# Kernel optimization log

Measured on AMD Instinct MI355X. Metric: run time of the kernel, lower is better.

The kernel has to match this reference:

```python
import jax, jax.numpy as jnp
import numpy as np
from jax.scipy.special import logsumexp

B, L = 32, 128
NEG = -1e9
SPAN_LAMB = 0.5


def setup_inputs() -> dict:
    key = jax.random.key(0)
    ks = jax.random.split(key, 8)
    span_logits = jax.random.normal(ks[0], (B, L, L, 2), jnp.float32)
    ph = jax.random.normal(ks[1], (B, L, L), jnp.float32)
    pt = jax.random.normal(ks[2], (B, L, L), jnp.float32)
    ph_arc = jax.random.normal(ks[3], (B, L, L), jnp.float32)
    spans_ind = jax.random.randint(ks[4], (B, L, L), 0, 3, jnp.int32)
    ph_ind = jax.random.randint(ks[5], (B, L, L), 0, 2, jnp.int32)
    pt_ind = jax.random.randint(ks[6], (B, L, L), 0, 2, jnp.int32)
    lens = jax.random.randint(ks[7], (B,), L // 2, L + 1, jnp.int32)
    i = jnp.arange(L)
    # maskspan[b,i,j] = valid right-closed span i..j within sentence b; row 0 sums to lens
    maskspan = (i[None, :, None] <= i[None, None, :]) & (i[None, None, :] < lens[:, None, None])
    maskarc = (i[None, :, None] < lens[:, None, None]) & (i[None, None, :] < lens[:, None, None])
    return dict(span_logits=span_logits, ph=ph, pt=pt, ph_arc=ph_arc,
                spans_ind=spans_ind, ph_ind=ph_ind, pt_ind=pt_ind,
                maskspan=maskspan, maskarc=maskarc)


def _inside_logZ(span_logits, lens):
    # CYK inside algorithm over right-closed spans; returns sum_b logZ_b.
    scores = logsumexp(span_logits, axis=-1)  # [B,L,L] span score = lse over labels
    Ln = scores.shape[1]
    ar = jnp.arange(Ln)
    # width-0 base: s[i,i] = scores[i,i]
    s0 = jnp.where(jnp.eye(Ln, dtype=bool)[None], scores, NEG)
    li = ar[:, None] + ar[None, :]        # [L,L]: left child right end i+k
    ri = li + 1                           # right child left end i+k+1
    li_c = jnp.clip(li, 0, Ln - 1)
    ri_c = jnp.clip(ri, 0, Ln - 1)

    def step(s, w):
        j = ar + w
        jc = jnp.clip(j, 0, Ln - 1)
        left = s[:, ar[:, None], li_c]                 # [B,L,L] left[b,i,k]=s[b,i,i+k]
        right = s[:, ri_c, jc[:, None]]                # right[b,i,k]=s[b,i+k+1,i+w]
        comb = jnp.where(ar[None, None, :] < w, left + right, NEG)
        new = scores[:, ar, jc] + logsumexp(comb, axis=-1)  # [B,L]
        valid = (j < Ln)[None, :]
        cur = s[:, ar, jc]
        s = s.at[:, ar, jc].set(jnp.where(valid, new, cur))
        return s, None

    s, _ = jax.lax.scan(step, s0, jnp.arange(1, Ln))
    logZ = jnp.take_along_axis(s[:, 0, :], (lens - 1)[:, None], axis=1)[:, 0]
    return logZ.sum()


def _bce_mean(x, y, m):
    # stable BCEWithLogits, mean over masked elements
    l = jnp.maximum(x, 0.0) - x * y + jnp.log1p(jnp.exp(-jnp.abs(x)))
    return jnp.where(m, l, 0.0).sum() / m.sum().astype(jnp.float32)


def reference(span_logits, ph, pt, ph_arc, spans_ind, ph_ind, pt_ind, maskspan, maskarc):
    lens = maskspan[:, 0].sum(-1)                         # [B]
    spans_b = jnp.where(spans_ind > 0, spans_ind - 1, spans_ind).astype(bool)
    # label marginals = d logZ / d span_logits (matches torch autograd-based cyk)
    marginals = jax.grad(_inside_logZ)(span_logits, lens)  # [B,L,L,2]
    pos_mask = maskspan & spans_b
    neg_mask = maskspan & (~spans_b)
    pos_loss = jnp.log(jnp.where(pos_mask, jnp.maximum(marginals[..., 1], 1e-38), 1.0)).sum()
    neg_loss = jnp.log(jnp.where(neg_mask, jnp.maximum(marginals[..., 0], 1e-38), 1.0)).sum()
    loss_spans = -(pos_loss + neg_loss) / lens.sum().astype(jnp.float32)
    loss_ph = _bce_mean(ph, ph_ind.astype(jnp.float32), maskarc)
    loss_pt = _bce_mean(pt, pt_ind.astype(jnp.float32), maskarc)
    return SPAN_LAMB * loss_spans + (1.0 - SPAN_LAMB) * (loss_ph + loss_pt)
```

## Files before the change

### kernel.cpp

```cpp
#include <hip/hip_runtime.h>
#include <hip/hip_bf16.h>
#include <float.h>

#define NB 32
#define NBCE 32
#define L 128
#define NT 1024
#define R 132
#define PAD 40
#define LOGMIN -87.49823f

__device__ __forceinline__ int mask_mode(const void* p) {
    unsigned int v = ((const unsigned int*)p)[0];
    if (v == 1u) return 1;
    if (v == 0x3F800000u) return 2;
    return 0;
}
__device__ __forceinline__ bool mask_at(const void* p, int mode, int idx) {
    if (mode == 1) return ((const int*)p)[idx] != 0;
    if (mode == 2) return ((const float*)p)[idx] != 0.0f;
    return ((const unsigned char*)p)[idx] != 0;
}

__device__ __forceinline__ float lse2(float a, float b) {
    return fmaxf(a, b) + log1pf(__expf(-fabsf(a - b)));
}

template<int C>
__device__ __forceinline__ float dppf(float x) {
    return __int_as_float(__builtin_amdgcn_mov_dpp(__float_as_int(x), C, 0xF, 0xF, true));
}
template<int T>
__device__ __forceinline__ float bfly_max(float x) {
    x = fmaxf(x, dppf<0xB1>(x));
    x = fmaxf(x, dppf<0x4E>(x));
    x = fmaxf(x, dppf<0x141>(x));
    if (T == 16) x = fmaxf(x, dppf<0x140>(x));
    return x;
}
template<int T>
__device__ __forceinline__ float bfly_add(float x) {
    x += dppf<0xB1>(x);
    x += dppf<0x4E>(x);
    x += dppf<0x141>(x);
    if (T == 16) x += dppf<0x140>(x);
    return x;
}

template<int T, int NUMAX>
__device__ __forceinline__ void load_terms(float* v, int sub, int nterm,
                                           const float* p1, const float* p2, float& mloc) {
    p1 += sub; p2 += sub;
#pragma unroll
    for (int kk = 0; kk < NUMAX; kk += 2) {
        if (kk * T >= nterm) break;
        const int o0 = kk * T, o1 = o0 + T;
        float a0 = p1[o0] + p2[o0];
        float a1 = p1[o1] + p2[o1];
        a0 = (sub + o0 < nterm) ? a0 : -FLT_MAX;
        a1 = (sub + o1 < nterm) ? a1 : -FLT_MAX;
        v[kk] = a0; v[kk + 1] = a1;
        mloc = fmaxf(mloc, fmaxf(a0, a1));
    }
}
template<int T, int NUMAX>
__device__ __forceinline__ void sum_exp(const float* v, int nterm, float M, float& s) {
#pragma unroll
    for (int kk = 0; kk < NUMAX; kk += 2) {
        if (kk * T >= nterm) break;
        s += __expf(v[kk] - M) + __expf(v[kk + 1] - M);
    }
}

__global__ __launch_bounds__(NT, 1) void tree_dp_kernel(
    const float* __restrict__ logits,
    const int*   __restrict__ spans_ind,
    const void*  __restrict__ maskspan,
    const float* __restrict__ ph, const float* __restrict__ pt,
    const int* __restrict__ ph_ind, const int* __restrict__ pt_ind,
    const void* __restrict__ maskarc,
    double*      __restrict__ ws)
{
    const int tid = threadIdx.x;

    if (blockIdx.x >= NB) {
        const int mode = mask_mode(maskarc);
        const int tot = NB * L * L;
        double sph = 0.0, spt = 0.0, cnt = 0.0;
        for (int idx = (blockIdx.x - NB) * NT + tid; idx < tot; idx += NBCE * NT) {
            if (mask_at(maskarc, mode, idx)) {
                float x = ph[idx]; float y = (float)ph_ind[idx];
                sph += (double)(fmaxf(x, 0.0f) - x * y + log1pf(__expf(-fabsf(x))));
                x = pt[idx]; y = (float)pt_ind[idx];
                spt += (double)(fmaxf(x, 0.0f) - x * y + log1pf(__expf(-fabsf(x))));
                cnt += 1.0;
            }
        }
        for (int off = 32; off > 0; off >>= 1) {
            sph += __shfl_down(sph, off);
            spt += __shfl_down(spt, off);
            cnt += __shfl_down(cnt, off);
        }
        if ((tid & 63) == 0) {
            atomicAdd(&ws[2], sph); atomicAdd(&ws[3], spt); atomicAdd(&ws[4], cnt);
        }
        return;
    }

    __shared__ float Am[L * R + PAD];
    __shared__ float Gm[L * R + PAD];

    const int b = blockIdx.x;
    const int mbase = b * L * L;
    const int mode = mask_mode(maskspan);

    int pred = (tid < L) && mask_at(maskspan, mode, mbase + tid);
    const int n = __syncthreads_count(pred);

    const float* lg = logits + (size_t)b * L * L * 2;

    for (int e = tid; e < L * L; e += NT) {
        int i = e >> 7, j = e & (L - 1);
        if (i <= j && j < n) {
            const float* p = lg + (size_t)e * 2;
            float v = lse2(p[0], p[1]);
            Am[i * R + j] = v; Am[j * R + i] = v;
            Gm[i * R + j] = v; Gm[j * R + i] = v;
        }
    }
    __syncthreads();

    for (int w = 1; w < n; ++w) {
        int c = n - w;
        if (c > 64) {
            int cell = tid >> 3, sub = tid & 7;
            if (cell < c) {
                int i = cell, j = i + w;
                float v[8]; float mloc = -FLT_MAX;
                load_terms<8, 8>(v, sub, w, &Am[i * R + i], &Am[j * R + i + 1], mloc);
                float M = bfly_max<8>(mloc);
                float s = 0.0f;
                sum_exp<8, 8>(v, w, M, s);
                float S = bfly_add<8>(s);
                if (sub == 0) {
                    float val = Am[i * R + j] + M + __logf(S);
                    Am[i * R + j] = val; Am[j * R + i] = val;
                }
            }
        } else {
            int cell = tid >> 4, sub = tid & 15;
            if (cell < c) {
                int i = cell, j = i + w;
                float v[8]; float mloc = -FLT_MAX;
                load_terms<16, 8>(v, sub, w, &Am[i * R + i], &Am[j * R + i + 1], mloc);
                float M = bfly_max<16>(mloc);
                float s = 0.0f;
                sum_exp<16, 8>(v, w, M, s);
                float S = bfly_add<16>(s);
                if (sub == 0) {
                    float val = Am[i * R + j] + M + __logf(S);
                    Am[i * R + j] = val; Am[j * R + i] = val;
                }
            }
        }
        __syncthreads();
    }

    const float logZ = Am[n - 1];

    for (int w = n - 2; w >= 1; --w) {
        int c = n - w;
        if (c > 64) {
            int cell = tid >> 3, sub = tid & 7;
            if (cell < c) {
                int i = cell, j = i + w;
                int nt1 = n - 1 - j;
                float v1[16], v2[16]; float mloc = -FLT_MAX;
                load_terms<8, 16>(v1, sub, nt1, &Gm[i * R + j + 1], &Am[(j + 1) * R + j + 1], mloc);
                load_terms<8, 16>(v2, sub, i,   &Gm[j * R],         &Am[(i - 1) * R],         mloc);
                float M = bfly_max<8>(mloc);
                float s = 0.0f;
                sum_exp<8, 16>(v1, nt1, M, s);
                sum_exp<8, 16>(v2, i,   M, s);
                float S = bfly_add<8>(s);
                if (sub == 0) {
                    float val = Gm[i * R + j] + M + __logf(S);
                    Gm[i * R + j] = val; Gm[j * R + i] = val;
                }
            }
        } else {
            int cell = tid >> 4, sub = tid & 15;
            if (cell < c) {
                int i = cell, j = i + w;
                int nt1 = n - 1 - j;
                float v1[4], v2[4]; float mloc = -FLT_MAX;
                load_terms<16, 4>(v1, sub, nt1, &Gm[i * R + j + 1], &Am[(j + 1) * R + j + 1], mloc);
                load_terms<16, 4>(v2, sub, i,   &Gm[j * R],         &Am[(i - 1) * R],         mloc);
                float M = bfly_max<16>(mloc);
                float s = 0.0f;
                sum_exp<16, 4>(v1, nt1, M, s);
                sum_exp<16, 4>(v2, i,   M, s);
                float S = bfly_add<16>(s);
                if (sub == 0) {
                    float val = Gm[i * R + j] + M + __logf(S);
                    Gm[i * R + j] = val; Gm[j * R + i] = val;
                }
            }
        }
        __syncthreads();
    }

    const int* si = spans_ind + mbase;
    double local = 0.0;
    {
        int cell = tid >> 3, sub = tid & 7;
        if (cell < n) {
            int i = cell;
            int nt1 = n - 1 - i;
            float v1[16], v2[16]; float mloc = -FLT_MAX;
            load_terms<8, 16>(v1, sub, nt1, &Gm[i * R + i + 1], &Am[(i + 1) * R + i + 1], mloc);
            load_terms<8, 16>(v2, sub, i,   &Gm[i * R],         &Am[(i - 1) * R],         mloc);
            float M = bfly_max<8>(mloc);
            float s = 0.0f;
            sum_exp<8, 16>(v1, nt1, M, s);
            sum_exp<8, 16>(v2, i,   M, s);
            float S = bfly_add<8>(s);
            if (sub == 0) {
                float beta_ii = M + __logf(S);
                const float* p = lg + ((size_t)i * L + i) * 2;
                int ind = si[i * L + i];
                float lc = (ind == 2) ? p[1] : p[0];
                float logm = beta_ii - logZ + lc;
                local += (double)fmaxf(logm, LOGMIN);
            }
        }
    }

    for (int e = tid; e < L * L; e += NT) {
        int i = e >> 7, j = e & (L - 1);
        if (i < j && j < n) {
            const float* p = lg + (size_t)e * 2;
            float a = p[0], cc = p[1];
            float sc = lse2(a, cc);
            int ind = si[e];
            float lc = (ind == 2) ? cc : a;
            float logm = Am[i * R + j] + Gm[i * R + j] - logZ + lc - 2.0f * sc;
            local += (double)fmaxf(logm, LOGMIN);
        }
    }

    for (int off = 32; off > 0; off >>= 1)
        local += __shfl_down(local, off);
    if ((tid & 63) == 0) atomicAdd(&ws[0], local);
    if (tid == 0) atomicAdd(&ws[1], (double)n);
}

__global__ void finalize_kernel(const double* __restrict__ ws, float* __restrict__ out) {
    double loss_spans = -ws[0] / ws[1];
    double bce = (ws[2] + ws[3]) / ws[4];
    out[0] = (float)(0.5 * loss_spans + 0.5 * bce);
}

extern "C" void kernel_launch(void* const* d_in, const int* in_sizes, int n_in,
                              void* d_out, int out_size, void* d_ws, size_t ws_size,
                              hipStream_t stream) {
    (void)in_sizes; (void)n_in; (void)out_size; (void)ws_size;
    const float* span_logits = (const float*)d_in[0];
    const float* ph          = (const float*)d_in[1];
    const float* pt          = (const float*)d_in[2];
    const int*   spans_ind   = (const int*)d_in[4];
    const int*   ph_ind      = (const int*)d_in[5];
    const int*   pt_ind      = (const int*)d_in[6];
    const void*  maskspan    = d_in[7];
    const void*  maskarc     = d_in[8];
    double* ws = (double*)d_ws;
    float* out = (float*)d_out;

    hipMemsetAsync(d_ws, 0, 5 * sizeof(double), stream);
    hipLaunchKernelGGL(tree_dp_kernel, dim3(NB + NBCE), dim3(NT), 0, stream,
                       span_logits, spans_ind, maskspan,
                       ph, pt, ph_ind, pt_ind, maskarc, ws);
    hipLaunchKernelGGL(finalize_kernel, dim3(1), dim3(1), 0, stream, ws, out);
}
```

Before: 323.7 us.

## Tile CYK inside/outside passes into 16x16 diagonal blocks with per-wave wavefront

Replaces the per-width global sweep (one block-wide barrier per span width, about n barriers each for inside and outside) with a 16x16 tiled schedule. For each tile diagonal, the split points outside the tile are reduced in bulk into a shared float2 buffer holding online-logsumexp pairs. Each wave then finishes its own tile with an intra-tile wavefront of 31 steps, using online max/sum merges and 4-lane DPP butterflies. This cuts block-level synchronizations to roughly 2·n/16, at the cost of more intra-wave serialized steps, extra shared memory, and changed floating-point summation order.

```diff
diff --git a/kernel.cpp b/kernel.cpp
--- a/kernel.cpp
+++ b/kernel.cpp
@@ -8,6 +8,7 @@
 #define NT 1024
 #define R 132
 #define PAD 40
+#define MAXD 8
 #define LOGMIN -87.49823f
 
 __device__ __forceinline__ int mask_mode(const void* p) {
@@ -26,9 +27,26 @@
     return fmaxf(a, b) + log1pf(__expf(-fabsf(a - b)));
 }
 
+__device__ __forceinline__ void lse_acc(float v, float& m, float& s) {
+    float nm = fmaxf(m, v);
+    s = s * __expf(m - nm) + __expf(v - nm);
+    m = nm;
+}
+__device__ __forceinline__ void lse_merge(float& m1, float& s1, float m2, float s2) {
+    float M = fmaxf(m1, m2);
+    s1 = s1 * __expf(m1 - M) + s2 * __expf(m2 - M);
+    m1 = M;
+}
+
 template<int C>
 __device__ __forceinline__ float dppf(float x) {
     return __int_as_float(__builtin_amdgcn_mov_dpp(__float_as_int(x), C, 0xF, 0xF, true));
+}
+__device__ __forceinline__ void bfly4_lse(float& m, float& s) {
+    float mo = dppf<0xB1>(m), so = dppf<0xB1>(s);
+    lse_merge(m, s, mo, so);
+    mo = dppf<0x4E>(m); so = dppf<0x4E>(s);
+    lse_merge(m, s, mo, so);
 }
 template<int T>
 __device__ __forceinline__ float bfly_max(float x) {
@@ -46,7 +64,6 @@
     if (T == 16) x += dppf<0x140>(x);
     return x;
 }
-
 template<int T, int NUMAX>
 __device__ __forceinline__ void load_terms(float* v, int sub, int nterm,
                                            const float* p1, const float* p2, float& mloc) {
@@ -109,6 +126,7 @@
 
     __shared__ float Am[L * R + PAD];
     __shared__ float Gm[L * R + PAD];
+    __shared__ float2 EB[MAXD * 256];
 
     const int b = blockIdx.x;
     const int mbase = b * L * L;
@@ -116,6 +134,7 @@
 
     int pred = (tid < L) && mask_at(maskspan, mode, mbase + tid);
     const int n = __syncthreads_count(pred);
+    const int D = (n + 15) >> 4;
 
     const float* lg = logits + (size_t)b * L * L * 2;
 
@@ -130,80 +149,145 @@
     }
     __syncthreads();
 
-    for (int w = 1; w < n; ++w) {
-        int c = n - w;
-        if (c > 64) {
-            int cell = tid >> 3, sub = tid & 7;
-            if (cell < c) {
-                int i = cell, j = i + w;
-                float v[8]; float mloc = -FLT_MAX;
-                load_terms<8, 8>(v, sub, w, &Am[i * R + i], &Am[j * R + i + 1], mloc);
-                float M = bfly_max<8>(mloc);
-                float s = 0.0f;
-                sum_exp<8, 8>(v, w, M, s);
-                float S = bfly_add<8>(s);
-                if (sub == 0) {
-                    float val = Am[i * R + j] + M + __logf(S);
-                    Am[i * R + j] = val; Am[j * R + i] = val;
-                }
-            }
-        } else {
-            int cell = tid >> 4, sub = tid & 15;
-            if (cell < c) {
-                int i = cell, j = i + w;
-                float v[8]; float mloc = -FLT_MAX;
-                load_terms<16, 8>(v, sub, w, &Am[i * R + i], &Am[j * R + i + 1], mloc);
-                float M = bfly_max<16>(mloc);
-                float s = 0.0f;
-                sum_exp<16, 8>(v, w, M, s);
-                float S = bfly_add<16>(s);
-                if (sub == 0) {
-                    float val = Am[i * R + j] + M + __logf(S);
-                    Am[i * R + j] = val; Am[j * R + i] = val;
-                }
-            }
+    const int wave = tid >> 6, lane = tid & 63;
+    const int cid4 = lane >> 2, sub4 = lane & 3;
+
+    if (wave < D) {
+        const int bI = wave << 4;
+        for (int lw = 1; lw < 16; ++lw) {
+            int li = cid4, lj = li + lw;
+            int i = bI + li, j = bI + lj;
+            bool act = (lj < 16) && (j < n);
+            float m0 = -FLT_MAX, s0 = 0.f;
+            if (act) {
+                const float* pL = Am + i * R + i;
+                const float* pR = Am + j * R + i + 1;
+                for (int t = sub4; t < lw; t += 4)
+                    lse_acc(pL[t] + pR[t], m0, s0);
+            }
+            bfly4_lse(m0, s0);
+            if (act && sub4 == 0) {
+                float v = Am[i * R + j] + m0 + __logf(s0);
+                Am[i * R + j] = v; Am[j * R + i] = v;
+            }
+        }
+    }
+    __syncthreads();
+
+    for (int d = 1; d < D; ++d) {
+        const int TD = D - d;
+        for (int cidx = tid; cidx < (TD << 8); cidx += NT) {
+            int It = cidx >> 8, c = cidx & 255;
+            int li = c >> 4, lj = c & 15;
+            int i = (It << 4) + li, j = ((It + d) << 4) + lj;
+            float m0 = -FLT_MAX, s0 = 0.f, m1 = -FLT_MAX, s1 = 0.f;
+            if (j < n) {
+                int mlo = (It << 4) + 15;
+                int cnt = (d << 4) - 15;
+                const float* p1 = Am + i * R + mlo;
+                const float* p2 = Am + j * R + mlo + 1;
+                int t = 0;
+                for (; t + 1 < cnt; t += 2) {
+                    lse_acc(p1[t] + p2[t], m0, s0);
+                    lse_acc(p1[t + 1] + p2[t + 1], m1, s1);
+                }
+                if (t < cnt) lse_acc(p1[t] + p2[t], m0, s0);
+                lse_merge(m0, s0, m1, s1);
+            }
+            EB[cidx] = make_float2(m0, s0);
         }
         __syncthreads();
+        if (wave < TD) {
+            const int bI = wave << 4, bJ = (wave + d) << 4;
+            const int ebase = wave << 8;
+            for (int step = 0; step < 31; ++step) {
+                int delta = step - 15;
+                int li = (delta >= 0) ? cid4 : (cid4 - delta);
+                int lj = li + delta;
+                int i = bI + li, j = bJ + lj;
+                bool act = (li < 16) && (lj < 16) && (j < n);
+                float m0 = -FLT_MAX, s0 = 0.f, m1 = -FLT_MAX, s1 = 0.f;
+                if (act) {
+                    const float* rI = Am + i * R;
+                    const float* rJ = Am + j * R;
+                    int nL = lj, nR = 15 - li;
+                    for (int t = sub4; t < nL; t += 4)
+                        lse_acc(rI[bJ + t] + rJ[bJ + 1 + t], m0, s0);
+                    for (int t = sub4; t < nR; t += 4)
+                        lse_acc(rI[bI + li + t] + rJ[bI + li + 1 + t], m1, s1);
+                    lse_merge(m0, s0, m1, s1);
+                }
+                bfly4_lse(m0, s0);
+                if (act && sub4 == 0) {
+                    float2 e = EB[ebase + (li << 4) + lj];
+                    lse_merge(m0, s0, e.x, e.y);
+                    float v = Am[i * R + j] + m0 + __logf(s0);
+                    Am[i * R + j] = v; Am[j * R + i] = v;
+                }
+            }
+        }
+        __syncthreads();
     }
 
     const float logZ = Am[n - 1];
 
-    for (int w = n - 2; w >= 1; --w) {
-        int c = n - w;
-        if (c > 64) {
-            int cell = tid >> 3, sub = tid & 7;
-            if (cell < c) {
-                int i = cell, j = i + w;
-                int nt1 = n - 1 - j;
-                float v1[16], v2[16]; float mloc = -FLT_MAX;
-                load_terms<8, 16>(v1, sub, nt1, &Gm[i * R + j + 1], &Am[(j + 1) * R + j + 1], mloc);
-                load_terms<8, 16>(v2, sub, i,   &Gm[j * R],         &Am[(i - 1) * R],         mloc);
-                float M = bfly_max<8>(mloc);
-                float s = 0.0f;
-                sum_exp<8, 16>(v1, nt1, M, s);
-                sum_exp<8, 16>(v2, i,   M, s);
-                float S = bfly_add<8>(s);
-                if (sub == 0) {
-                    float val = Gm[i * R + j] + M + __logf(S);
-                    Gm[i * R + j] = val; Gm[j * R + i] = val;
-                }
-            }
-        } else {
-            int cell = tid >> 4, sub = tid & 15;
-            if (cell < c) {
-                int i = cell, j = i + w;
-                int nt1 = n - 1 - j;
-                float v1[4], v2[4]; float mloc = -FLT_MAX;
-                load_terms<16, 4>(v1, sub, nt1, &Gm[i * R + j + 1], &Am[(j + 1) * R + j + 1], mloc);
-                load_terms<16, 4>(v2, sub, i,   &Gm[j * R],         &Am[(i - 1) * R],         mloc);
-                float M = bfly_max<16>(mloc);
-                float s = 0.0f;
-                sum_exp<16, 4>(v1, nt1, M, s);
-                sum_exp<16, 4>(v2, i,   M, s);
-                float S = bfly_add<16>(s);
-                if (sub == 0) {
-                    float val = Gm[i * R + j] + M + __logf(S);
-                    Gm[i * R + j] = val; Gm[j * R + i] = val;
+    for (int d = D - 1; d >= 0; --d) {
+        const int TD = D - d;
+        for (int cidx = tid; cidx < (TD << 8); cidx += NT) {
+            int It = cidx >> 8, c = cidx & 255;
+            int li = c >> 4, lj = c & 15;
+            int I = It, J = It + d;
+            int i = (I << 4) + li, j = (J << 4) + lj;
+            float m0 = -FLT_MAX, s0 = 0.f, m1 = -FLT_MAX, s1 = 0.f;
+            if (j < n) {
+                int k0 = (J + 1) << 4;
+                int nEA = n - k0; if (nEA < 0) nEA = 0;
+                int t = 0;
+                for (; t + 1 < nEA; t += 2) {
+                    lse_acc(Gm[i * R + k0 + t] + Am[(j + 1) * R + k0 + t], m0, s0);
+                    lse_acc(Gm[i * R + k0 + t + 1] + Am[(j + 1) * R + k0 + t + 1], m1, s1);
+                }
+                if (t < nEA) lse_acc(Gm[i * R + k0 + t] + Am[(j + 1) * R + k0 + t], m0, s0);
+                int nEB_ = I << 4;
+                t = 0;
+                for (; t + 1 < nEB_; t += 2) {
+                    lse_acc(Gm[j * R + t] + Am[(i - 1) * R + t], m0, s0);
+                    lse_acc(Gm[j * R + t + 1] + Am[(i - 1) * R + t + 1], m1, s1);
+                }
+                if (t < nEB_) lse_acc(Gm[j * R + t] + Am[(i - 1) * R + t], m0, s0);
+                lse_merge(m0, s0, m1, s1);
+            }
+            EB[cidx] = make_float2(m0, s0);
+        }
+        __syncthreads();
+        if (wave < TD) {
+            const int bI = wave << 4, bJ = (wave + d) << 4;
+            const int ebase = wave << 8;
+            const int stepLo = (d == 0) ? 16 : 0;
+            for (int step = 30; step >= stepLo; --step) {
+                int delta = step - 15;
+                int li = (delta >= 0) ? cid4 : (cid4 - delta);
+                int lj = li + delta;
+                int i = bI + li, j = bJ + lj;
+                bool act = (li < 16) && (lj < 16) && (j < n);
+                float m0 = -FLT_MAX, s0 = 0.f, m1 = -FLT_MAX, s1 = 0.f;
+                if (act) {
+                    int nA = 15 - lj; { int lim = n - 1 - j; if (nA > lim) nA = lim; }
+                    int nB = li;
+                    for (int t = sub4; t < nA; t += 4)
+                        lse_acc(Gm[i * R + j + 1 + t] + Am[(j + 1) * R + j + 1 + t], m0, s0);
+                    for (int t = sub4; t < nB; t += 4)
+                        lse_acc(Gm[j * R + bI + t] + Am[(i - 1) * R + bI + t], m1, s1);
+                    lse_merge(m0, s0, m1, s1);
+                }
+                bfly4_lse(m0, s0);
+                if (act && sub4 == 0) {
+                    float2 e = EB[ebase + (li << 4) + lj];
+                    lse_merge(m0, s0, e.x, e.y);
+                    if (s0 > 0.f) {
+                        float v = Gm[i * R + j] + m0 + __logf(s0);
+                        Gm[i * R + j] = v; Gm[j * R + i] = v;
+                    }
                 }
             }
         }
@@ -235,7 +319,6 @@
             }
         }
     }
-
     for (int e = tid; e < L * L; e += NT) {
         int i = e >> 7, j = e & (L - 1);
         if (i < j && j < n) {
@@ -248,7 +331,6 @@
             local += (double)fmaxf(logm, LOGMIN);
         }
     }
-
     for (int off = 32; off > 0; off >>= 1)
         local += __shfl_down(local, off);
     if ((tid & 63) == 0) atomicAdd(&ws[0], local);
```

After: 551.9 us. 70.5% more time.

## Overlap wavefront steps by deferring edge-dependent terms past the barrier

Applied to the files above, without the earlier changes.

Each step of the inside and outside wavefronts now reduces only the terms that do not depend on the previous width before the barrier. The two boundary terms that read cells from the immediately preceding width are folded in afterwards with an online log-sum-exp update. That leaves one barrier per width while letting most of the reduction for width w run alongside the tail writes of width w-1. The risk is subtle ordering bugs, since the post-barrier writes of one step race with the pre-barrier reads of the next step.

```diff
diff --git a/kernel.cpp b/kernel.cpp
--- a/kernel.cpp
+++ b/kernel.cpp
@@ -26,6 +26,12 @@
     return fmaxf(a, b) + log1pf(__expf(-fabsf(a - b)));
 }
 
+__device__ __forceinline__ void lse_acc(float v, float& m, float& s) {
+    float nm = fmaxf(m, v);
+    s = s * __expf(m - nm) + __expf(v - nm);
+    m = nm;
+}
+
 template<int C>
 __device__ __forceinline__ float dppf(float x) {
     return __int_as_float(__builtin_amdgcn_mov_dpp(__float_as_int(x), C, 0xF, 0xF, true));
@@ -46,7 +52,6 @@
     if (T == 16) x += dppf<0x140>(x);
     return x;
 }
-
 template<int T, int NUMAX>
 __device__ __forceinline__ void load_terms(float* v, int sub, int nterm,
                                            const float* p1, const float* p2, float& mloc) {
@@ -130,85 +135,116 @@
     }
     __syncthreads();
 
-    for (int w = 1; w < n; ++w) {
+    if (tid < n - 1) {
+        int i = tid, j = i + 1;
+        float val = Am[i * R + j] + Am[i * R + i] + Am[j * R + j];
+        Am[i * R + j] = val; Am[j * R + i] = val;
+    }
+
+    for (int w = 2; w < n; ++w) {
         int c = n - w;
+        float M = -FLT_MAX, S = 0.0f;
+        float pre_sc = 0.f, pre_di = 0.f, pre_dj = 0.f;
+        int i = 0, j = 0, sub = 0; bool act = false; bool lead = false;
+        int nb = w - 2;
         if (c > 64) {
-            int cell = tid >> 3, sub = tid & 7;
-            if (cell < c) {
-                int i = cell, j = i + w;
+            int cell = tid >> 3; sub = tid & 7;
+            act = cell < c;
+            if (act) {
+                i = cell; j = i + w;
                 float v[8]; float mloc = -FLT_MAX;
-                load_terms<8, 8>(v, sub, w, &Am[i * R + i], &Am[j * R + i + 1], mloc);
-                float M = bfly_max<8>(mloc);
+                load_terms<8, 8>(v, sub, nb, &Am[i * R + i + 1], &Am[j * R + i + 2], mloc);
+                M = bfly_max<8>(mloc);
                 float s = 0.0f;
-                sum_exp<8, 8>(v, w, M, s);
-                float S = bfly_add<8>(s);
-                if (sub == 0) {
-                    float val = Am[i * R + j] + M + __logf(S);
-                    Am[i * R + j] = val; Am[j * R + i] = val;
-                }
+                sum_exp<8, 8>(v, nb, M, s);
+                S = bfly_add<8>(s);
             }
         } else {
-            int cell = tid >> 4, sub = tid & 15;
-            if (cell < c) {
-                int i = cell, j = i + w;
+            int cell = tid >> 4; sub = tid & 15;
+            act = cell < c;
+            if (act) {
+                i = cell; j = i + w;
                 float v[8]; float mloc = -FLT_MAX;
-                load_terms<16, 8>(v, sub, w, &Am[i * R + i], &Am[j * R + i + 1], mloc);
-                float M = bfly_max<16>(mloc);
+                load_terms<16, 8>(v, sub, nb, &Am[i * R + i + 1], &Am[j * R + i + 2], mloc);
+                M = bfly_max<16>(mloc);
                 float s = 0.0f;
-                sum_exp<16, 8>(v, w, M, s);
-                float S = bfly_add<16>(s);
-                if (sub == 0) {
-                    float val = Am[i * R + j] + M + __logf(S);
-                    Am[i * R + j] = val; Am[j * R + i] = val;
-                }
-            }
+                sum_exp<16, 8>(v, nb, M, s);
+                S = bfly_add<16>(s);
+            }
+        }
+        lead = act && (sub == 0);
+        if (lead) {
+            pre_sc = Am[i * R + j];
+            pre_di = Am[i * R + i];
+            pre_dj = Am[j * R + j];
         }
         __syncthreads();
-    }
+        if (lead) {
+            float f1 = pre_di + Am[j * R + i + 1];
+            float f2 = Am[i * R + j - 1] + pre_dj;
+            lse_acc(f1, M, S);
+            lse_acc(f2, M, S);
+            float val = pre_sc + M + __logf(S);
+            Am[i * R + j] = val; Am[j * R + i] = val;
+        }
+    }
+    __syncthreads();
 
     const float logZ = Am[n - 1];
 
     for (int w = n - 2; w >= 1; --w) {
         int c = n - w;
+        float M = -FLT_MAX, S = 0.0f;
+        float pre_sc = 0.f, pre_aj = 0.f, pre_ai = 0.f;
+        int i = 0, j = 0, sub = 0; bool act = false; bool lead = false;
         if (c > 64) {
-            int cell = tid >> 3, sub = tid & 7;
-            if (cell < c) {
-                int i = cell, j = i + w;
-                int nt1 = n - 1 - j;
+            int cell = tid >> 3; sub = tid & 7;
+            act = cell < c;
+            if (act) {
+                i = cell; j = i + w;
+                int nA = n - j - 2; if (nA < 0) nA = 0;
+                int nB = i - 1;     if (nB < 0) nB = 0;
                 float v1[16], v2[16]; float mloc = -FLT_MAX;
-                load_terms<8, 16>(v1, sub, nt1, &Gm[i * R + j + 1], &Am[(j + 1) * R + j + 1], mloc);
-                load_terms<8, 16>(v2, sub, i,   &Gm[j * R],         &Am[(i - 1) * R],         mloc);
-                float M = bfly_max<8>(mloc);
+                load_terms<8, 16>(v1, sub, nA, &Gm[i * R + j + 2], &Am[(j + 1) * R + j + 2], mloc);
+                load_terms<8, 16>(v2, sub, nB, &Gm[j * R],         &Am[(i - 1) * R],         mloc);
+                M = bfly_max<8>(mloc);
                 float s = 0.0f;
-                sum_exp<8, 16>(v1, nt1, M, s);
-                sum_exp<8, 16>(v2, i,   M, s);
-                float S = bfly_add<8>(s);
-                if (sub == 0) {
-                    float val = Gm[i * R + j] + M + __logf(S);
-                    Gm[i * R + j] = val; Gm[j * R + i] = val;
-                }
+                sum_exp<8, 16>(v1, nA, M, s);
+                sum_exp<8, 16>(v2, nB, M, s);
+                S = bfly_add<8>(s);
             }
         } else {
-            int cell = tid >> 4, sub = tid & 15;
-            if (cell < c) {
-                int i = cell, j = i + w;
-                int nt1 = n - 1 - j;
+            int cell = tid >> 4; sub = tid & 15;
+            act = cell < c;
+            if (act) {
+                i = cell; j = i + w;
+                int nA = n - j - 2; if (nA < 0) nA = 0;
+                int nB = i - 1;     if (nB < 0) nB = 0;
                 float v1[4], v2[4]; float mloc = -FLT_MAX;
-                load_terms<16, 4>(v1, sub, nt1, &Gm[i * R + j + 1], &Am[(j + 1) * R + j + 1], mloc);
-                load_terms<16, 4>(v2, sub, i,   &Gm[j * R],         &Am[(i - 1) * R],         mloc);
-                float M = bfly_max<16>(mloc);
+                load_terms<16, 4>(v1, sub, nA, &Gm[i * R + j + 2], &Am[(j + 1) * R + j + 2], mloc);
+                load_terms<16, 4>(v2, sub, nB, &Gm[j * R],         &Am[(i - 1) * R],         mloc);
+                M = bfly_max<16>(mloc);
                 float s = 0.0f;
-                sum_exp<16, 4>(v1, nt1, M, s);
-                sum_exp<16, 4>(v2, i,   M, s);
-                float S = bfly_add<16>(s);
-                if (sub == 0) {
-                    float val = Gm[i * R + j] + M + __logf(S);
-                    Gm[i * R + j] = val; Gm[j * R + i] = val;
-                }
-            }
+                sum_exp<16, 4>(v1, nA, M, s);
+                sum_exp<16, 4>(v2, nB, M, s);
+                S = bfly_add<16>(s);
+            }
+        }
+        lead = act && (sub == 0);
+        if (lead) {
+            pre_sc = Gm[i * R + j];
+            pre_aj = (j < n - 1) ? Am[(j + 1) * R + j + 1] : 0.f;
+            pre_ai = (i > 0)     ? Am[(i - 1) * R + i - 1] : 0.f;
         }
         __syncthreads();
-    }
+        if (lead) {
+            if (j < n - 1) lse_acc(Gm[i * R + j + 1] + pre_aj, M, S);
+            if (i > 0)     lse_acc(Gm[(i - 1) * R + j] + pre_ai, M, S);
+            float val = pre_sc + M + __logf(S);
+            Gm[i * R + j] = val; Gm[j * R + i] = val;
+        }
+    }
+    __syncthreads();
 
     const int* si = spans_ind + mbase;
     double local = 0.0;
@@ -235,7 +271,6 @@
             }
         }
     }
-
     for (int e = tid; e < L * L; e += NT) {
         int i = e >> 7, j = e & (L - 1);
         if (i < j && j < n) {
@@ -248,7 +283,6 @@
             local += (double)fmaxf(logm, LOGMIN);
         }
     }
-
     for (int off = 32; off > 0; off >>= 1)
         local += __shfl_down(local, off);
     if ((tid & 63) == 0) atomicAdd(&ws[0], local);
```

After: 364.2 us. 12.5% more time.
